# Performance work log

Hardware: AMD Instinct MI355X
Metric: run time of the kernel (lower is better)

Reference implementation:

```python
import jax, jax.numpy as jnp
import numpy as np

N_NODES = 100000
N_EDGES = 1600000
IN_DIM = 128
OUT_DIM = 64
HEADS = 4
NEG_SLOPE = 0.2  # PyG GATConv default
LN_EPS = 1e-5


def setup_inputs() -> dict:
    key = jax.random.key(0)
    ks = jax.random.split(key, 8)
    x = jax.random.normal(ks[0], (N_NODES, IN_DIM), dtype=jnp.float32)
    edge_index = jax.random.randint(ks[1], (2, N_EDGES), 0, N_NODES, dtype=jnp.int64)
    # GATConv params: lin weight, per-head attention vectors, output bias (concat=False)
    s = 1.0 / np.sqrt(IN_DIM)
    W = jax.random.uniform(ks[2], (IN_DIM, HEADS * OUT_DIM), jnp.float32, -s, s)
    att_src = jax.random.uniform(ks[3], (HEADS, OUT_DIM), jnp.float32, -s, s)
    att_dst = jax.random.uniform(ks[4], (HEADS, OUT_DIM), jnp.float32, -s, s)
    bias = jnp.zeros((OUT_DIM,), jnp.float32)
    gamma = jnp.ones((OUT_DIM,), jnp.float32)
    beta = jnp.zeros((OUT_DIM,), jnp.float32)
    return {"x": x, "edge_index": edge_index, "W": W, "att_src": att_src,
            "att_dst": att_dst, "bias": bias, "gamma": gamma, "beta": beta}


def reference(x, edge_index, W, att_src, att_dst, bias, gamma, beta):
    N = x.shape[0]
    H, C = att_src.shape
    # Linear projection, split heads: (N, H, C)
    xl = (x @ W).reshape(N, H, C)
    # Per-node attention logits: (N, H)
    a_src = jnp.einsum('nhc,hc->nh', xl, att_src)
    a_dst = jnp.einsum('nhc,hc->nh', xl, att_dst)
    # Add self-loops (PyG GATConv default add_self_loops=True)
    loops = jnp.arange(N, dtype=edge_index.dtype)
    src = jnp.concatenate([edge_index[0], loops])  # (E+N,)
    dst = jnp.concatenate([edge_index[1], loops])
    # Per-edge attention: gather, leaky_relu, segment softmax over destination
    alpha = jax.nn.leaky_relu(a_src[src] + a_dst[dst], NEG_SLOPE)  # (E+N, H)
    amax = jax.ops.segment_max(alpha, dst, num_segments=N)  # (N, H)
    e = jnp.exp(alpha - amax[dst])
    denom = jax.ops.segment_sum(e, dst, num_segments=N)  # (N, H)
    alpha = e / (denom[dst] + 1e-16)
    # Message passing: scatter-add alpha-weighted source features to dst
    msg = xl[src] * alpha[:, :, None]  # (E+N, H, C)
    out = jax.ops.segment_sum(msg, dst, num_segments=N)  # (N, H, C)
    out = out.mean(axis=1) + bias  # concat=False -> head average, (N, C)
    # LayerNorm
    mu = out.mean(axis=-1, keepdims=True)
    var = out.var(axis=-1, keepdims=True)
    return (out - mu) * jax.lax.rsqrt(var + LN_EPS) * gamma + beta
```

## Files before the change

### kernel.cpp

```cpp
#include <hip/hip_runtime.h>
#include <hip/hip_fp16.h>

#define IN_DIM   128
#define HC       256
#define OUT_DIM  64
#define HEADS    4
#define NEG_SLOPE 0.2f
#define LN_EPS   1e-5f
#define MAXBINS  512
#define SCAT_TPE 16

typedef short bf16x8 __attribute__((ext_vector_type(8)));
typedef float f32x4  __attribute__((ext_vector_type(4)));

__device__ __forceinline__ float lrelu(float a){ return a > 0.f ? a : NEG_SLOPE * a; }

__device__ __forceinline__ unsigned short f2bf(float f){
  unsigned u = __float_as_uint(f);
  u = u + 0x7fffu + ((u >> 16) & 1u);
  return (unsigned short)(u >> 16);
}
__device__ __forceinline__ unsigned pk2(float a, float b){
  return (unsigned)f2bf(a) | ((unsigned)f2bf(b) << 16);
}
__device__ __forceinline__ __half2 u2h(unsigned u){ return *(__half2*)&u; }
__device__ __forceinline__ unsigned h2u(__half2 h){ return *(unsigned*)&h; }

__device__ __forceinline__ float wsum(float v){
  #pragma unroll
  for (int o = 32; o; o >>= 1) v += __shfl_xor(v, o);
  return v;
}

__device__ __forceinline__ bool detect32(const int* ei){
  int ln = threadIdx.x & 63;
  unsigned probe = (ln < 32) ? (unsigned)ei[2*ln + 1] : 0u;
  return __ballot(probe != 0) != 0ull;
}

__global__ void k_prep(const float* __restrict__ W, unsigned short* __restrict__ Wt,
                       int* bincnt){
  int n = blockIdx.x;
  int k = threadIdx.x;
  Wt[n*IN_DIM + k] = f2bf(W[k*HC + n]);
  int i = blockIdx.x*blockDim.x + threadIdx.x;
  if (i < MAXBINS) bincnt[i] = 0;
}

__global__ __launch_bounds__(256) void k_gemm_mfma(
    const float* __restrict__ x, const unsigned short* __restrict__ Wt,
    const float* __restrict__ att_s, const float* __restrict__ att_d,
    __half* __restrict__ xl_t, float* __restrict__ a_src,
    float* __restrict__ a_dst, int N)
{
  __shared__ unsigned short sxa[64*IN_DIM];
  __shared__ unsigned short sxl[64*HC];
  int t = threadIdx.x;
  int nb = blockIdx.x * 64;

  #pragma unroll
  for (int it = 0; it < 4; ++it){
    int idx = it*256 + t;
    int row = idx >> 4, seg = idx & 15;
    uint4 pk = make_uint4(0,0,0,0);
    if (nb + row < N){
      const float* xr = x + (size_t)(nb + row)*IN_DIM + seg*8;
      float4 f0 = *(const float4*)xr;
      float4 f1 = *(const float4*)(xr + 4);
      pk.x = pk2(f0.x, f0.y); pk.y = pk2(f0.z, f0.w);
      pk.z = pk2(f1.x, f1.y); pk.w = pk2(f1.z, f1.w);
    }
    int byte = (row*256 + seg*16) ^ ((row & 7) << 4);
    *(uint4*)((char*)sxa + byte) = pk;
  }
  __syncthreads();

  int w = t >> 6, l = t & 63;

  bf16x8 bfr[4][4];
  #pragma unroll
  for (int nt = 0; nt < 4; ++nt){
    int col = w*64 + nt*16 + (l & 15);
    #pragma unroll
    for (int ks = 0; ks < 4; ++ks)
      bfr[nt][ks] = *(const bf16x8*)(Wt + (size_t)col*IN_DIM + ks*32 + ((l >> 4) << 3));
  }
  float attS[4], attD[4];
  #pragma unroll
  for (int nt = 0; nt < 4; ++nt){
    attS[nt] = att_s[w*64 + nt*16 + (l & 15)];
    attD[nt] = att_d[w*64 + nt*16 + (l & 15)];
  }

  #pragma unroll
  for (int sub = 0; sub < 4; ++sub){
    bf16x8 afr[4];
    #pragma unroll
    for (int ks = 0; ks < 4; ++ks){
      int row = sub*16 + (l & 15);
      int byte = (row*256 + ks*64 + ((l >> 4) << 4)) ^ ((row & 7) << 4);
      afr[ks] = *(const bf16x8*)((const char*)sxa + byte);
    }
    f32x4 acc[4] = {{0,0,0,0},{0,0,0,0},{0,0,0,0},{0,0,0,0}};
    #pragma unroll
    for (int nt = 0; nt < 4; ++nt)
      #pragma unroll
      for (int ks = 0; ks < 4; ++ks)
        acc[nt] = __builtin_amdgcn_mfma_f32_16x16x32_bf16(afr[ks], bfr[nt][ks], acc[nt], 0, 0, 0);

    #pragma unroll
    for (int r = 0; r < 4; ++r){
      float ps = 0.f, pd = 0.f;
      #pragma unroll
      for (int nt = 0; nt < 4; ++nt){
        ps = fmaf(acc[nt][r], attS[nt], ps);
        pd = fmaf(acc[nt][r], attD[nt], pd);
      }
      #pragma unroll
      for (int o = 8; o; o >>= 1){ ps += __shfl_xor(ps, o); pd += __shfl_xor(pd, o); }
      int node = nb + sub*16 + (l >> 4)*4 + r;
      if ((l & 15) == 0 && node < N){
        a_src[node*4 + w] = ps;
        a_dst[node*4 + w] = pd;
      }
    }

    #pragma unroll
    for (int nt = 0; nt < 4; ++nt){
      int ch = nt*16 + (l & 15);
      #pragma unroll
      for (int r = 0; r < 4; ++r){
        int row = sub*16 + (l >> 4)*4 + r;
        sxl[row*HC + ch*4 + w] = __half_as_ushort(__float2half(acc[nt][r]));
      }
    }
  }
  __syncthreads();
  const uint4* s4 = (const uint4*)sxl;
  uint4* g4 = (uint4*)(xl_t + (size_t)nb*HC);
  for (int c = t; c < 2048; c += 256){
    int row = c >> 5;
    if (nb + row < N) g4[c] = s4[c];
  }
}


__global__ __launch_bounds__(256) void k_bincount(const int* ei, int* bincnt,
                                                  int E, int nbins){
  __shared__ int h[MAXBINS];
  bool i32 = detect32(ei);
  for (int i = threadIdx.x; i < nbins; i += 256) h[i] = 0;
  __syncthreads();
  int idx = blockIdx.x*blockDim.x + threadIdx.x;
  int stride = gridDim.x*blockDim.x;
  for (int e = idx; e < E; e += stride){
    int d = i32 ? ei[E + e] : (int)((const long long*)ei)[(size_t)E + e];
    atomicAdd(&h[d >> 8], 1);
  }
  __syncthreads();
  for (int i = threadIdx.x; i < nbins; i += 256)
    if (h[i]) atomicAdd(&bincnt[i], h[i]);
}

__global__ __launch_bounds__(512) void k_binscan(const int* __restrict__ bincnt,
    int* binstart, int* bincur, int* rowstart, int nbins, int N, int E){
  __shared__ int sh[512];
  int tid = threadIdx.x;
  int v = (tid < nbins) ? bincnt[tid] : 0;
  sh[tid] = v; __syncthreads();
  #pragma unroll
  for (int off = 1; off < 512; off <<= 1){
    int t = (tid >= off) ? sh[tid-off] : 0;
    __syncthreads();
    sh[tid] += t;
    __syncthreads();
  }
  int ex = sh[tid] - v;
  if (tid < nbins){ binstart[tid] = ex; bincur[tid] = ex; }
  if (tid == 0){ binstart[nbins] = E; rowstart[N] = E; }
}

__global__ __launch_bounds__(256) void k_binscatter(const int* ei, int* bincur,
    unsigned* tmp, int E, int nbins){
  __shared__ int h[MAXBINS];
  __shared__ int base[MAXBINS];
  bool i32 = detect32(ei);
  int tile0 = blockIdx.x * (256*SCAT_TPE);
  for (int i = threadIdx.x; i < nbins; i += 256) h[i] = 0;
  __syncthreads();
  unsigned pk[SCAT_TPE]; int rk[SCAT_TPE];
  #pragma unroll
  for (int k = 0; k < SCAT_TPE; ++k){
    int e = tile0 + k*256 + threadIdx.x;
    if (e < E){
      int s, d;
      if (i32){ s = ei[e]; d = ei[E + e]; }
      else {
        s = (int)((const long long*)ei)[e];
        d = (int)((const long long*)ei)[(size_t)E + e];
      }
      int b = d >> 8;
      pk[k] = (unsigned)s | ((unsigned)(d & 255) << 20);
      rk[k] = atomicAdd(&h[b], 1) | (b << 16);
    }
  }
  __syncthreads();
  for (int i = threadIdx.x; i < nbins; i += 256)
    base[i] = h[i] ? atomicAdd(&bincur[i], h[i]) : 0;
  __syncthreads();
  #pragma unroll
  for (int k = 0; k < SCAT_TPE; ++k){
    int e = tile0 + k*256 + threadIdx.x;
    if (e < E){
      int b = rk[k] >> 16, r = rk[k] & 0xFFFF;
      tmp[base[b] + r] = pk[k];
    }
  }
}

__global__ __launch_bounds__(256) void k_binsort(const unsigned* __restrict__ tmp,
    const int* __restrict__ binstart, int* rowstart, int* csr, int N){
  __shared__ int c[256], c2[256], sc[256];
  int b = blockIdx.x, tid = threadIdx.x;
  int s0 = binstart[b], s1 = binstart[b+1];
  c[tid] = 0; c2[tid] = 0;
  __syncthreads();
  for (int e = s0 + tid; e < s1; e += 256)
    atomicAdd(&c[(tmp[e] >> 20) & 255], 1);
  __syncthreads();
  int v = c[tid]; sc[tid] = v;
  __syncthreads();
  #pragma unroll
  for (int off = 1; off < 256; off <<= 1){
    int t = (tid >= off) ? sc[tid-off] : 0;
    __syncthreads();
    sc[tid] += t;
    __syncthreads();
  }
  int ex = sc[tid] - v;
  int d = b*256 + tid;
  if (d < N) rowstart[d] = s0 + ex;
  sc[tid] = ex;
  __syncthreads();
  for (int e = s0 + tid; e < s1; e += 256){
    unsigned u = tmp[e];
    int dl = (u >> 20) & 255;
    int pos = s0 + sc[dl] + atomicAdd(&c2[dl], 1);
    csr[pos] = (int)(u & 0xFFFFFu);
  }
}

__global__ __launch_bounds__(256) void k_node(
    const int* __restrict__ rowstart, const int* __restrict__ csr,
    const float4* __restrict__ a_src4, const float4* __restrict__ a_dst4,
    const __half* __restrict__ xl_t,
    const float* __restrict__ bias, const float* __restrict__ gamma,
    const float* __restrict__ beta, float* __restrict__ out, int N)
{
  __shared__ uint2 wlds[4][64];
  __shared__ int   slds[4][64];
  int wv = threadIdx.x >> 6, ln = threadIdx.x & 63;
  int node = blockIdx.x*4 + wv;
  if (node >= N) return;
  int g = ln >> 4, i = ln & 15;

  int start = rowstart[node], end = rowstart[node+1];
  float4 ad = a_dst4[node];
  float4 asl = a_src4[node];

  float es0 = __expf(lrelu(asl.x + ad.x));
  float es1 = __expf(lrelu(asl.y + ad.y));
  float es2 = __expf(lrelu(asl.z + ad.z));
  float es3 = __expf(lrelu(asl.w + ad.w));

  __half2 acc[8];
  #pragma unroll
  for (int m = 0; m < 8; ++m) acc[m] = __float2half2_rn(0.f);
  float lp0 = 0.f, lp1 = 0.f, lp2 = 0.f, lp3 = 0.f;

  for (int t = start; t < end; t += 64){
    int nt = end - t; if (nt > 64) nt = 64;
    int sid = 0;
    float e0 = 0.f, e1 = 0.f, e2 = 0.f, e3 = 0.f;
    if (ln < nt){
      sid = csr[t + ln];
      float4 as4 = a_src4[sid];
      e0 = __expf(lrelu(as4.x + ad.x));
      e1 = __expf(lrelu(as4.y + ad.y));
      e2 = __expf(lrelu(as4.z + ad.z));
      e3 = __expf(lrelu(as4.w + ad.w));
      lp0 += e0; lp1 += e1; lp2 += e2; lp3 += e3;
    }
    wlds[wv][ln] = make_uint2(h2u(__floats2half2_rn(e0, e1)),
                              h2u(__floats2half2_rn(e2, e3)));
    slds[wv][ln] = sid;

    int nwin = (nt + 3) >> 2;
    for (int j = 0; j < nwin; ++j){
      int e = j*4 + g;
      uint2 wpk = wlds[wv][e];
      int sj = slds[wv][e];
      __half2 w01 = u2h(wpk.x), w23 = u2h(wpk.y);
      const uint4* p = (const uint4*)((const char*)xl_t + ((size_t)sj*512 + (i << 5)));
      uint4 xa = p[0], xb = p[1];
      acc[0] = __hfma2(w01, u2h(xa.x), acc[0]);
      acc[1] = __hfma2(w23, u2h(xa.y), acc[1]);
      acc[2] = __hfma2(w01, u2h(xa.z), acc[2]);
      acc[3] = __hfma2(w23, u2h(xa.w), acc[3]);
      acc[4] = __hfma2(w01, u2h(xb.x), acc[4]);
      acc[5] = __hfma2(w23, u2h(xb.y), acc[5]);
      acc[6] = __hfma2(w01, u2h(xb.z), acc[6]);
      acc[7] = __hfma2(w23, u2h(xb.w), acc[7]);
    }
  }

  #pragma unroll
  for (int m = 0; m < 8; ++m){
    acc[m] = __hadd2(acc[m], u2h(__shfl_xor(h2u(acc[m]), 16)));
    acc[m] = __hadd2(acc[m], u2h(__shfl_xor(h2u(acc[m]), 32)));
  }

  {
    __half2 s01 = __floats2half2_rn(es0, es1);
    __half2 s23 = __floats2half2_rn(es2, es3);
    const uint4* p = (const uint4*)((const char*)xl_t + ((size_t)node*512 + (i << 5)));
    uint4 xa = p[0], xb = p[1];
    acc[0] = __hfma2(s01, u2h(xa.x), acc[0]);
    acc[1] = __hfma2(s23, u2h(xa.y), acc[1]);
    acc[2] = __hfma2(s01, u2h(xa.z), acc[2]);
    acc[3] = __hfma2(s23, u2h(xa.w), acc[3]);
    acc[4] = __hfma2(s01, u2h(xb.x), acc[4]);
    acc[5] = __hfma2(s23, u2h(xb.y), acc[5]);
    acc[6] = __hfma2(s01, u2h(xb.z), acc[6]);
    acc[7] = __hfma2(s23, u2h(xb.w), acc[7]);
  }

  __half2 lp01 = __floats2half2_rn(lp0, lp1);
  __half2 lp23 = __floats2half2_rn(lp2, lp3);
  #pragma unroll
  for (int o = 32; o; o >>= 1){
    lp01 = __hadd2(lp01, u2h(__shfl_xor(h2u(lp01), o)));
    lp23 = __hadd2(lp23, u2h(__shfl_xor(h2u(lp23), o)));
  }
  float r0 = __builtin_amdgcn_rcpf(__low2float(lp01) + es0);
  float r1 = __builtin_amdgcn_rcpf(__high2float(lp01) + es1);
  float r2 = __builtin_amdgcn_rcpf(__low2float(lp23) + es2);
  float r3 = __builtin_amdgcn_rcpf(__high2float(lp23) + es3);

  float4 b4 = *(const float4*)(bias + 4*i);
  float o0 = 0.25f*(__low2float(acc[0])*r0 + __high2float(acc[0])*r1 +
                    __low2float(acc[1])*r2 + __high2float(acc[1])*r3) + b4.x;
  float o1 = 0.25f*(__low2float(acc[2])*r0 + __high2float(acc[2])*r1 +
                    __low2float(acc[3])*r2 + __high2float(acc[3])*r3) + b4.y;
  float o2 = 0.25f*(__low2float(acc[4])*r0 + __high2float(acc[4])*r1 +
                    __low2float(acc[5])*r2 + __high2float(acc[5])*r3) + b4.z;
  float o3 = 0.25f*(__low2float(acc[6])*r0 + __high2float(acc[6])*r1 +
                    __low2float(acc[7])*r2 + __high2float(acc[7])*r3) + b4.w;

  float s  = wsum(o0 + o1 + o2 + o3) * 0.25f;
  float sq = wsum(o0*o0 + o1*o1 + o2*o2 + o3*o3) * 0.25f;
  float mu = s * (1.f/OUT_DIM);
  float var = sq * (1.f/OUT_DIM) - mu*mu;
  float rs = rsqrtf(var + LN_EPS);
  float4 g4v = *(const float4*)(gamma + 4*i);
  float4 be4 = *(const float4*)(beta + 4*i);
  if (ln < 16){
    float4 ov;
    ov.x = (o0 - mu)*rs*g4v.x + be4.x;
    ov.y = (o1 - mu)*rs*g4v.y + be4.y;
    ov.z = (o2 - mu)*rs*g4v.z + be4.z;
    ov.w = (o3 - mu)*rs*g4v.w + be4.w;
    *(float4*)(out + (size_t)node*OUT_DIM + 4*i) = ov;
  }
}

extern "C" void kernel_launch(void* const* d_in, const int* in_sizes, int n_in,
                              void* d_out, int out_size, void* d_ws, size_t ws_size,
                              hipStream_t stream)
{
  const float* x     = (const float*)d_in[0];
  const int*   ei    = (const int*)d_in[1];
  const float* W     = (const float*)d_in[2];
  const float* att_s = (const float*)d_in[3];
  const float* att_d = (const float*)d_in[4];
  const float* bias  = (const float*)d_in[5];
  const float* gamma = (const float*)d_in[6];
  const float* beta  = (const float*)d_in[7];
  float* out = (float*)d_out;

  int N = in_sizes[0] / IN_DIM;
  int E = in_sizes[1] / 2;
  int nbins = (N + 255) >> 8;

  char* ws = (char*)d_ws;
  __half* xl_t = (__half*)ws;                   ws += (size_t)N*HC*sizeof(__half);
  float* a_src = (float*)ws;                    ws += (size_t)N*HEADS*sizeof(float);
  float* a_dst = (float*)ws;                    ws += (size_t)N*HEADS*sizeof(float);
  int* rowstart = (int*)ws;                     ws += ((size_t)N+1)*sizeof(int);
  int* csr      = (int*)ws;                     ws += (size_t)E*sizeof(int);
  unsigned* tmp = (unsigned*)ws;                ws += (size_t)E*sizeof(unsigned);
  int* bincnt   = (int*)ws;                     ws += MAXBINS*sizeof(int);
  int* binstart = (int*)ws;                     ws += (MAXBINS+1)*sizeof(int);
  int* bincur   = (int*)ws;                     ws += MAXBINS*sizeof(int);
  unsigned short* Wt = (unsigned short*)ws;     ws += (size_t)HC*IN_DIM*sizeof(unsigned short);

  k_prep     <<<HC, IN_DIM, 0, stream>>>(W, Wt, bincnt);
  k_gemm_mfma<<<(N + 63)/64, 256, 0, stream>>>(x, Wt, att_s, att_d, xl_t, a_src, a_dst, N);
  k_bincount <<<1024, 256, 0, stream>>>(ei, bincnt, E, nbins);
  k_binscan  <<<1, 512, 0, stream>>>(bincnt, binstart, bincur, rowstart, nbins, N, E);
  k_binscatter<<<(E + 256*SCAT_TPE - 1)/(256*SCAT_TPE), 256, 0, stream>>>(ei, bincur, tmp, E, nbins);
  k_binsort  <<<nbins, 256, 0, stream>>>(tmp, binstart, rowstart, csr, N);
  k_node     <<<(N + 3)/4, 256, 0, stream>>>(rowstart, csr,
               (const float4*)a_src, (const float4*)a_dst, xl_t,
               bias, gamma, beta, out, N);
}
```

Measured before the change: 248.8 us.

## Fuse GEMM with bin scatter kernel and map four nodes per wavefront

The GEMM and the edge bin-scatter stages now run as one launch, with the block index choosing which body a block executes. This lets the independent projection work and the CSR construction overlap instead of running back to back. The node aggregation kernel now handles four destination nodes per wavefront, 16 lanes each, rather than one node per wave. Each node walks its edges in chunks of 16 with a wave-wide max trip count, and the self-loop term seeds the accumulator. This targets idle lanes on low-degree nodes, at the cost of divergence when degrees differ within a wave and a 48KB shared buffer for the fused kernel.

Measured after the change: 238.6 us. 4.1% less time.

```diff
diff --git a/kernel.cpp b/kernel.cpp
--- a/kernel.cpp
+++ b/kernel.cpp
@@ -26,12 +26,6 @@
 __device__ __forceinline__ __half2 u2h(unsigned u){ return *(__half2*)&u; }
 __device__ __forceinline__ unsigned h2u(__half2 h){ return *(unsigned*)&h; }
 
-__device__ __forceinline__ float wsum(float v){
-  #pragma unroll
-  for (int o = 32; o; o >>= 1) v += __shfl_xor(v, o);
-  return v;
-}
-
 __device__ __forceinline__ bool detect32(const int* ei){
   int ln = threadIdx.x & 63;
   unsigned probe = (ln < 32) ? (unsigned)ei[2*ln + 1] : 0u;
@@ -47,16 +41,16 @@
   if (i < MAXBINS) bincnt[i] = 0;
 }
 
-__global__ __launch_bounds__(256) void k_gemm_mfma(
+__device__ __forceinline__ void gemm_body(int bid, char* smem,
     const float* __restrict__ x, const unsigned short* __restrict__ Wt,
     const float* __restrict__ att_s, const float* __restrict__ att_d,
     __half* __restrict__ xl_t, float* __restrict__ a_src,
     float* __restrict__ a_dst, int N)
 {
-  __shared__ unsigned short sxa[64*IN_DIM];
-  __shared__ unsigned short sxl[64*HC];
+  unsigned short* sxa = (unsigned short*)smem;
+  unsigned short* sxl = (unsigned short*)(smem + 16384);
   int t = threadIdx.x;
-  int nb = blockIdx.x * 64;
+  int nb = bid * 64;
 
   #pragma unroll
   for (int it = 0; it < 4; ++it){
@@ -71,7 +65,7 @@
       pk.z = pk2(f1.x, f1.y); pk.w = pk2(f1.z, f1.w);
     }
     int byte = (row*256 + seg*16) ^ ((row & 7) << 4);
-    *(uint4*)((char*)sxa + byte) = pk;
+    *(uint4*)(smem + byte) = pk;
   }
   __syncthreads();
 
@@ -99,7 +93,7 @@
     for (int ks = 0; ks < 4; ++ks){
       int row = sub*16 + (l & 15);
       int byte = (row*256 + ks*64 + ((l >> 4) << 4)) ^ ((row & 7) << 4);
-      afr[ks] = *(const bf16x8*)((const char*)sxa + byte);
+      afr[ks] = *(const bf16x8*)(smem + byte);
     }
     f32x4 acc[4] = {{0,0,0,0},{0,0,0,0},{0,0,0,0},{0,0,0,0}};
     #pragma unroll
@@ -144,48 +138,13 @@
   }
 }
 
-
-__global__ __launch_bounds__(256) void k_bincount(const int* ei, int* bincnt,
-                                                  int E, int nbins){
-  __shared__ int h[MAXBINS];
+__device__ __forceinline__ void scat_body(int bid, char* smem,
+    const int* ei, int* bincur, unsigned* tmp, int E, int nbins)
+{
+  int* h    = (int*)smem;
+  int* base = (int*)(smem + 2048);
   bool i32 = detect32(ei);
-  for (int i = threadIdx.x; i < nbins; i += 256) h[i] = 0;
-  __syncthreads();
-  int idx = blockIdx.x*blockDim.x + threadIdx.x;
-  int stride = gridDim.x*blockDim.x;
-  for (int e = idx; e < E; e += stride){
-    int d = i32 ? ei[E + e] : (int)((const long long*)ei)[(size_t)E + e];
-    atomicAdd(&h[d >> 8], 1);
-  }
-  __syncthreads();
-  for (int i = threadIdx.x; i < nbins; i += 256)
-    if (h[i]) atomicAdd(&bincnt[i], h[i]);
-}
-
-__global__ __launch_bounds__(512) void k_binscan(const int* __restrict__ bincnt,
-    int* binstart, int* bincur, int* rowstart, int nbins, int N, int E){
-  __shared__ int sh[512];
-  int tid = threadIdx.x;
-  int v = (tid < nbins) ? bincnt[tid] : 0;
-  sh[tid] = v; __syncthreads();
-  #pragma unroll
-  for (int off = 1; off < 512; off <<= 1){
-    int t = (tid >= off) ? sh[tid-off] : 0;
-    __syncthreads();
-    sh[tid] += t;
-    __syncthreads();
-  }
-  int ex = sh[tid] - v;
-  if (tid < nbins){ binstart[tid] = ex; bincur[tid] = ex; }
-  if (tid == 0){ binstart[nbins] = E; rowstart[N] = E; }
-}
-
-__global__ __launch_bounds__(256) void k_binscatter(const int* ei, int* bincur,
-    unsigned* tmp, int E, int nbins){
-  __shared__ int h[MAXBINS];
-  __shared__ int base[MAXBINS];
-  bool i32 = detect32(ei);
-  int tile0 = blockIdx.x * (256*SCAT_TPE);
+  int tile0 = bid * (256*SCAT_TPE);
   for (int i = threadIdx.x; i < nbins; i += 256) h[i] = 0;
   __syncthreads();
   unsigned pk[SCAT_TPE]; int rk[SCAT_TPE];
@@ -218,6 +177,56 @@
   }
 }
 
+__global__ __launch_bounds__(256) void k_gemm_scat(
+    const float* __restrict__ x, const unsigned short* __restrict__ Wt,
+    const float* __restrict__ att_s, const float* __restrict__ att_d,
+    __half* __restrict__ xl_t, float* __restrict__ a_src, float* __restrict__ a_dst,
+    int N, const int* ei, int* bincur, unsigned* tmp, int E, int nbins,
+    int gemmBlocks)
+{
+  __shared__ char smem[49152];
+  int bid = (int)blockIdx.x;
+  if (bid < gemmBlocks)
+    gemm_body(bid, smem, x, Wt, att_s, att_d, xl_t, a_src, a_dst, N);
+  else
+    scat_body(bid - gemmBlocks, smem, ei, bincur, tmp, E, nbins);
+}
+
+__global__ __launch_bounds__(256) void k_bincount(const int* ei, int* bincnt,
+                                                  int E, int nbins){
+  __shared__ int h[MAXBINS];
+  bool i32 = detect32(ei);
+  for (int i = threadIdx.x; i < nbins; i += 256) h[i] = 0;
+  __syncthreads();
+  int idx = blockIdx.x*blockDim.x + threadIdx.x;
+  int stride = gridDim.x*blockDim.x;
+  for (int e = idx; e < E; e += stride){
+    int d = i32 ? ei[E + e] : (int)((const long long*)ei)[(size_t)E + e];
+    atomicAdd(&h[d >> 8], 1);
+  }
+  __syncthreads();
+  for (int i = threadIdx.x; i < nbins; i += 256)
+    if (h[i]) atomicAdd(&bincnt[i], h[i]);
+}
+
+__global__ __launch_bounds__(512) void k_binscan(const int* __restrict__ bincnt,
+    int* binstart, int* bincur, int* rowstart, int nbins, int N, int E){
+  __shared__ int sh[512];
+  int tid = threadIdx.x;
+  int v = (tid < nbins) ? bincnt[tid] : 0;
+  sh[tid] = v; __syncthreads();
+  #pragma unroll
+  for (int off = 1; off < 512; off <<= 1){
+    int t = (tid >= off) ? sh[tid-off] : 0;
+    __syncthreads();
+    sh[tid] += t;
+    __syncthreads();
+  }
+  int ex = sh[tid] - v;
+  if (tid < nbins){ binstart[tid] = ex; bincur[tid] = ex; }
+  if (tid == 0){ binstart[nbins] = E; rowstart[N] = E; }
+}
+
 __global__ __launch_bounds__(256) void k_binsort(const unsigned* __restrict__ tmp,
     const int* __restrict__ binstart, int* rowstart, int* csr, int N){
   __shared__ int c[256], c2[256], sc[256];
@@ -257,33 +266,51 @@
     const float* __restrict__ bias, const float* __restrict__ gamma,
     const float* __restrict__ beta, float* __restrict__ out, int N)
 {
-  __shared__ uint2 wlds[4][64];
-  __shared__ int   slds[4][64];
+  __shared__ uint2 wlds[4][4][16];
+  __shared__ int   slds[4][4][16];
   int wv = threadIdx.x >> 6, ln = threadIdx.x & 63;
-  int node = blockIdx.x*4 + wv;
-  if (node >= N) return;
   int g = ln >> 4, i = ln & 15;
-
-  int start = rowstart[node], end = rowstart[node+1];
-  float4 ad = a_dst4[node];
-  float4 asl = a_src4[node];
+  int node = blockIdx.x*16 + wv*4 + g;
+  bool alive = node < N;
+  int nc = alive ? node : N-1;
+
+  int start = rowstart[nc];
+  int end   = alive ? rowstart[nc+1] : start;
+  float4 ad  = a_dst4[nc];
+  float4 asl = a_src4[nc];
 
   float es0 = __expf(lrelu(asl.x + ad.x));
   float es1 = __expf(lrelu(asl.y + ad.y));
   float es2 = __expf(lrelu(asl.z + ad.z));
   float es3 = __expf(lrelu(asl.w + ad.w));
 
+  __half2 s01 = __floats2half2_rn(es0, es1);
+  __half2 s23 = __floats2half2_rn(es2, es3);
+  const uint4* ps = (const uint4*)((const char*)xl_t + ((size_t)nc*512 + (i << 5)));
+  uint4 xa = ps[0], xb = ps[1];
   __half2 acc[8];
-  #pragma unroll
-  for (int m = 0; m < 8; ++m) acc[m] = __float2half2_rn(0.f);
+  acc[0] = __hmul2(s01, u2h(xa.x));
+  acc[1] = __hmul2(s23, u2h(xa.y));
+  acc[2] = __hmul2(s01, u2h(xa.z));
+  acc[3] = __hmul2(s23, u2h(xa.w));
+  acc[4] = __hmul2(s01, u2h(xb.x));
+  acc[5] = __hmul2(s23, u2h(xb.y));
+  acc[6] = __hmul2(s01, u2h(xb.z));
+  acc[7] = __hmul2(s23, u2h(xb.w));
   float lp0 = 0.f, lp1 = 0.f, lp2 = 0.f, lp3 = 0.f;
 
-  for (int t = start; t < end; t += 64){
-    int nt = end - t; if (nt > 64) nt = 64;
+  for (int t = start; ; t += 16){
+    int rem = end - t;
+    rem = rem < 0 ? 0 : (rem > 16 ? 16 : rem);
+    int rmax = rem;
+    rmax = max(rmax, __shfl_xor(rmax, 16));
+    rmax = max(rmax, __shfl_xor(rmax, 32));
+    if (rmax == 0) break;
+
     int sid = 0;
     float e0 = 0.f, e1 = 0.f, e2 = 0.f, e3 = 0.f;
-    if (ln < nt){
-      sid = csr[t + ln];
+    if (i < rem){
+      sid = csr[t + i];
       float4 as4 = a_src4[sid];
       e0 = __expf(lrelu(as4.x + ad.x));
       e1 = __expf(lrelu(as4.y + ad.y));
@@ -291,54 +318,34 @@
       e3 = __expf(lrelu(as4.w + ad.w));
       lp0 += e0; lp1 += e1; lp2 += e2; lp3 += e3;
     }
-    wlds[wv][ln] = make_uint2(h2u(__floats2half2_rn(e0, e1)),
-                              h2u(__floats2half2_rn(e2, e3)));
-    slds[wv][ln] = sid;
-
-    int nwin = (nt + 3) >> 2;
-    for (int j = 0; j < nwin; ++j){
-      int e = j*4 + g;
-      uint2 wpk = wlds[wv][e];
-      int sj = slds[wv][e];
-      __half2 w01 = u2h(wpk.x), w23 = u2h(wpk.y);
-      const uint4* p = (const uint4*)((const char*)xl_t + ((size_t)sj*512 + (i << 5)));
-      uint4 xa = p[0], xb = p[1];
-      acc[0] = __hfma2(w01, u2h(xa.x), acc[0]);
-      acc[1] = __hfma2(w23, u2h(xa.y), acc[1]);
-      acc[2] = __hfma2(w01, u2h(xa.z), acc[2]);
-      acc[3] = __hfma2(w23, u2h(xa.w), acc[3]);
-      acc[4] = __hfma2(w01, u2h(xb.x), acc[4]);
-      acc[5] = __hfma2(w23, u2h(xb.y), acc[5]);
-      acc[6] = __hfma2(w01, u2h(xb.z), acc[6]);
-      acc[7] = __hfma2(w23, u2h(xb.w), acc[7]);
-    }
-  }
-
-  #pragma unroll
-  for (int m = 0; m < 8; ++m){
-    acc[m] = __hadd2(acc[m], u2h(__shfl_xor(h2u(acc[m]), 16)));
-    acc[m] = __hadd2(acc[m], u2h(__shfl_xor(h2u(acc[m]), 32)));
-  }
-
-  {
-    __half2 s01 = __floats2half2_rn(es0, es1);
-    __half2 s23 = __floats2half2_rn(es2, es3);
-    const uint4* p = (const uint4*)((const char*)xl_t + ((size_t)node*512 + (i << 5)));
-    uint4 xa = p[0], xb = p[1];
-    acc[0] = __hfma2(s01, u2h(xa.x), acc[0]);
-    acc[1] = __hfma2(s23, u2h(xa.y), acc[1]);
-    acc[2] = __hfma2(s01, u2h(xa.z), acc[2]);
-    acc[3] = __hfma2(s23, u2h(xa.w), acc[3]);
-    acc[4] = __hfma2(s01, u2h(xb.x), acc[4]);
-    acc[5] = __hfma2(s23, u2h(xb.y), acc[5]);
-    acc[6] = __hfma2(s01, u2h(xb.z), acc[6]);
-    acc[7] = __hfma2(s23, u2h(xb.w), acc[7]);
+    wlds[wv][g][i] = make_uint2(h2u(__floats2half2_rn(e0, e1)),
+                                h2u(__floats2half2_rn(e2, e3)));
+    slds[wv][g][i] = sid;
+
+    #pragma unroll 2
+    for (int j = 0; j < rmax; ++j){
+      if (j < rem){
+        uint2 wpk = wlds[wv][g][j];
+        int sj = slds[wv][g][j];
+        __half2 w01 = u2h(wpk.x), w23 = u2h(wpk.y);
+        const uint4* p = (const uint4*)((const char*)xl_t + ((size_t)sj*512 + (i << 5)));
+        uint4 ya = p[0], yb = p[1];
+        acc[0] = __hfma2(w01, u2h(ya.x), acc[0]);
+        acc[1] = __hfma2(w23, u2h(ya.y), acc[1]);
+        acc[2] = __hfma2(w01, u2h(ya.z), acc[2]);
+        acc[3] = __hfma2(w23, u2h(ya.w), acc[3]);
+        acc[4] = __hfma2(w01, u2h(yb.x), acc[4]);
+        acc[5] = __hfma2(w23, u2h(yb.y), acc[5]);
+        acc[6] = __hfma2(w01, u2h(yb.z), acc[6]);
+        acc[7] = __hfma2(w23, u2h(yb.w), acc[7]);
+      }
+    }
   }
 
   __half2 lp01 = __floats2half2_rn(lp0, lp1);
   __half2 lp23 = __floats2half2_rn(lp2, lp3);
   #pragma unroll
-  for (int o = 32; o; o >>= 1){
+  for (int o = 8; o; o >>= 1){
     lp01 = __hadd2(lp01, u2h(__shfl_xor(h2u(lp01), o)));
     lp23 = __hadd2(lp23, u2h(__shfl_xor(h2u(lp23), o)));
   }
@@ -357,14 +364,19 @@
   float o3 = 0.25f*(__low2float(acc[6])*r0 + __high2float(acc[6])*r1 +
                     __low2float(acc[7])*r2 + __high2float(acc[7])*r3) + b4.w;
 
-  float s  = wsum(o0 + o1 + o2 + o3) * 0.25f;
-  float sq = wsum(o0*o0 + o1*o1 + o2*o2 + o3*o3) * 0.25f;
+  float s  = o0 + o1 + o2 + o3;
+  float sq = o0*o0 + o1*o1 + o2*o2 + o3*o3;
+  #pragma unroll
+  for (int o = 8; o; o >>= 1){
+    s  += __shfl_xor(s, o);
+    sq += __shfl_xor(sq, o);
+  }
   float mu = s * (1.f/OUT_DIM);
   float var = sq * (1.f/OUT_DIM) - mu*mu;
   float rs = rsqrtf(var + LN_EPS);
   float4 g4v = *(const float4*)(gamma + 4*i);
   float4 be4 = *(const float4*)(beta + 4*i);
-  if (ln < 16){
+  if (alive){
     float4 ov;
     ov.x = (o0 - mu)*rs*g4v.x + be4.x;
     ov.y = (o1 - mu)*rs*g4v.y + be4.y;
@@ -404,13 +416,17 @@
   int* bincur   = (int*)ws;                     ws += MAXBINS*sizeof(int);
   unsigned short* Wt = (unsigned short*)ws;     ws += (size_t)HC*IN_DIM*sizeof(unsigned short);
 
-  k_prep     <<<HC, IN_DIM, 0, stream>>>(W, Wt, bincnt);
-  k_gemm_mfma<<<(N + 63)/64, 256, 0, stream>>>(x, Wt, att_s, att_d, xl_t, a_src, a_dst, N);
-  k_bincount <<<1024, 256, 0, stream>>>(ei, bincnt, E, nbins);
-  k_binscan  <<<1, 512, 0, stream>>>(bincnt, binstart, bincur, rowstart, nbins, N, E);
-  k_binscatter<<<(E + 256*SCAT_TPE - 1)/(256*SCAT_TPE), 256, 0, stream>>>(ei, bincur, tmp, E, nbins);
-  k_binsort  <<<nbins, 256, 0, stream>>>(tmp, binstart, rowstart, csr, N);
-  k_node     <<<(N + 3)/4, 256, 0, stream>>>(rowstart, csr,
-               (const float4*)a_src, (const float4*)a_dst, xl_t,
-               bias, gamma, beta, out, N);
-}
+  int gemmBlocks = (N + 63)/64;
+  int scatBlocks = (E + 256*SCAT_TPE - 1)/(256*SCAT_TPE);
+
+  k_prep    <<<HC, IN_DIM, 0, stream>>>(W, Wt, bincnt);
+  k_bincount<<<1024, 256, 0, stream>>>(ei, bincnt, E, nbins);
+  k_binscan <<<1, 512, 0, stream>>>(bincnt, binstart, bincur, rowstart, nbins, N, E);
+  k_gemm_scat<<<gemmBlocks + scatBlocks, 256, 0, stream>>>(
+      x, Wt, att_s, att_d, xl_t, a_src, a_dst, N, ei, bincur, tmp, E, nbins,
+      gemmBlocks);
+  k_binsort <<<nbins, 256, 0, stream>>>(tmp, binstart, rowstart, csr, N);
+  k_node    <<<(N + 15)/16, 256, 0, stream>>>(rowstart, csr,
+              (const float4*)a_src, (const float4*)a_dst, xl_t,
+              bias, gamma, beta, out, N);
+}
```
